# Performance work log

Measured on AMD Instinct MI355X. Metric: run time of the kernel, lower is better.

The kernel has to match this reference:

```python
import jax, jax.numpy as jnp
import numpy as np

N, E, D, G, L = 100_000, 500_000, 128, 512, 4
BN_EPS = 1e-5

def _bn(v, g, b):
    # BatchNorm1d in training mode: biased batch stats over node/graph axis
    m = v.mean(0)
    var = v.var(0)
    return (v - m) * jax.lax.rsqrt(var + BN_EPS) * g + b

def setup_inputs() -> dict:
    key = jax.random.key(0)
    ks = jax.random.split(key, 12)
    s = 0.05
    return {
        "x": jax.random.normal(ks[0], (N, D), jnp.float32),
        "edge_index": jax.random.randint(ks[1], (2, E), 0, N, jnp.int64),
        "batch": jnp.sort(jax.random.randint(ks[2], (N,), 0, G, jnp.int64)),
        "num_graphs": G,
        "W1": jax.random.normal(ks[3], (L, D, 2 * D), jnp.float32) * s,
        "b1": jnp.zeros((L, 2 * D), jnp.float32),
        "g1": jnp.ones((L, 2 * D), jnp.float32),
        "be1": jnp.zeros((L, 2 * D), jnp.float32),
        "W2": jax.random.normal(ks[4], (L, 2 * D, D), jnp.float32) * s,
        "b2": jnp.zeros((L, D), jnp.float32),
        "gbn": jnp.ones((L, D), jnp.float32),
        "bbn": jnp.zeros((L, D), jnp.float32),
        "eps": jnp.zeros((L,), jnp.float32),
        "cW1": jax.random.normal(ks[5], (3 * D, D), jnp.float32) * s,
        "cb1": jnp.zeros((D,), jnp.float32),
        "cg": jnp.ones((D,), jnp.float32),
        "cbeta": jnp.zeros((D,), jnp.float32),
        "cW2": jax.random.normal(ks[6], (D, D // 2), jnp.float32) * s,
        "cb2": jnp.zeros((D // 2,), jnp.float32),
        "cW3": jax.random.normal(ks[7], (D // 2, 2), jnp.float32) * s,
        "cb3": jnp.zeros((2,), jnp.float32),
    }

def reference(x, edge_index, batch, num_graphs, W1, b1, g1, be1, W2, b2, gbn, bbn, eps,
              cW1, cb1, cg, cbeta, cW2, cb2, cW3, cb3):
    n = x.shape[0]
    src, dst = edge_index[0], edge_index[1]
    for l in range(W1.shape[0]):
        # GINConv: mlp((1+eps)*x + sum_{j in N(i)} x_j)  (scatter-add to dst)
        agg = jax.ops.segment_sum(x[src], dst, num_segments=n)
        h = (1.0 + eps[l]) * x + agg
        h = jax.nn.relu(_bn(h @ W1[l] + b1[l], g1[l], be1[l]))
        h = h @ W2[l] + b2[l]
        x = jax.nn.relu(_bn(h, gbn[l], bbn[l]))  # outer BN + ReLU (dropout off: eval)
    # multi-pool readout: add / mean / max per graph
    s = jax.ops.segment_sum(x, batch, num_segments=num_graphs)
    cnt = jax.ops.segment_sum(jnp.ones((n,), x.dtype), batch, num_segments=num_graphs)
    mean = s / jnp.maximum(cnt, 1.0)[:, None]
    mx = jax.ops.segment_max(x, batch, num_segments=num_graphs)
    z = jnp.concatenate([s, mean, mx], axis=-1)  # [G, 3*D]
    z = jax.nn.relu(_bn(z @ cW1 + cb1, cg, cbeta))
    z = jax.nn.relu(z @ cW2 + cb2)
    return z @ cW3 + cb3
```

## Files before the change

### kernel.cpp

```cpp
#include <hip/hip_runtime.h>
#include <cstdint>
#include <cstddef>

#define NN 100000
#define EE 500000
#define DD 128
#define GG 512
#define LL 4
#define BN_EPS 1e-5f

typedef __attribute__((ext_vector_type(8))) short short8;
typedef __attribute__((ext_vector_type(8))) unsigned short ushort8v;
typedef __attribute__((ext_vector_type(4))) float f32x4;

static __device__ __forceinline__ unsigned short f2bf(float f) {
  union { float f; unsigned u; } v;
  v.f = f;
  unsigned r = v.u + 0x7fffu + ((v.u >> 16) & 1u);
  return (unsigned short)(r >> 16);
}
static __device__ __forceinline__ float bf2f(unsigned short u) {
  union { unsigned u; float f; } v;
  v.u = ((unsigned)u) << 16;
  return v.f;
}


__global__ void k_hist(const int* __restrict__ ei, int* __restrict__ cnt) {
  int e = blockIdx.x * 256 + threadIdx.x;
  if (e < EE) {
    int d = ei[EE + e];
    if (d >= 0 && d < NN) atomicAdd(&cnt[d], 1);
  }
}

__global__ void k_part(const int* __restrict__ cnt, int* __restrict__ part) {
  __shared__ int sm[1024];
  int t = threadIdx.x;
  int i = blockIdx.x * 1024 + t;
  sm[t] = (i < NN) ? cnt[i] : 0;
  __syncthreads();
  for (int off = 512; off > 0; off >>= 1) {
    if (t < off) sm[t] += sm[t + off];
    __syncthreads();
  }
  if (t == 0) part[blockIdx.x] = sm[0];
}

__global__ void k_scanpart(const int* __restrict__ part, int* __restrict__ partx, int nb) {
  __shared__ int sm[128];
  int t = threadIdx.x;
  int v = (t < nb) ? part[t] : 0;
  sm[t] = v;
  __syncthreads();
  for (int off = 1; off < 128; off <<= 1) {
    int u = (t >= off) ? sm[t - off] : 0;
    __syncthreads();
    sm[t] += u;
    __syncthreads();
  }
  if (t < nb) partx[t] = sm[t] - v;
}

__global__ void k_rs(const int* __restrict__ cnt, const int* __restrict__ partx,
                     int* __restrict__ rs, int* __restrict__ cur) {
  __shared__ int sm[1024];
  int t = threadIdx.x;
  int i = blockIdx.x * 1024 + t;
  int v = (i < NN) ? cnt[i] : 0;
  sm[t] = v;
  __syncthreads();
  for (int off = 1; off < 1024; off <<= 1) {
    int u = (t >= off) ? sm[t - off] : 0;
    __syncthreads();
    sm[t] += u;
    __syncthreads();
  }
  if (i < NN) {
    int excl = partx[blockIdx.x] + sm[t] - v;
    rs[i] = excl;
    cur[i] = excl;
    if (i == NN - 1) rs[NN] = excl + v;
  }
}

__global__ void k_fill(const int* __restrict__ ei, int* __restrict__ cur,
                       int* __restrict__ ci) {
  int e = blockIdx.x * 256 + threadIdx.x;
  if (e < EE) {
    int s = ei[e];
    int d = ei[EE + e];
    if (d >= 0 && d < NN && s >= 0 && s < NN) {
      int pos = atomicAdd(&cur[d], 1);
      if (pos >= 0 && pos < EE) ci[pos] = s;
    }
  }
}


__global__ void k_conv(const float* __restrict__ W1, const float* __restrict__ W2,
                       unsigned short* __restrict__ W1t, unsigned short* __restrict__ W2t) {
  int idx = blockIdx.x * 256 + threadIdx.x;
  if (idx < 4 * 256 * 128) {
    {
      int l = idx >> 15, rem = idx & 32767;
      int nc = rem >> 7, k = rem & 127;
      W1t[idx] = f2bf(W1[(l << 15) + k * 256 + nc]);
    }
    {
      int l = idx >> 15, rem = idx & 32767;
      int nc = rem >> 8, k = rem & 255;
      W2t[idx] = f2bf(W2[(l << 15) + k * 128 + nc]);
    }
  }
}


__global__ void k_x2bf(const float* __restrict__ x, unsigned short* __restrict__ xb) {
  int i = blockIdx.x * 256 + threadIdx.x;
  if (i < NN * DD / 4) {
    float4 v = *(const float4*)(x + (size_t)i * 4);
    ushort4 o;
    o.x = f2bf(v.x); o.y = f2bf(v.y); o.z = f2bf(v.z); o.w = f2bf(v.w);
    *(ushort4*)(xb + (size_t)i * 4) = o;
  }
}


__global__ __launch_bounds__(256) void k_agg_bf16(
    const unsigned short* __restrict__ X, const int* __restrict__ rs,
    const int* __restrict__ ci, const float* __restrict__ epsv, int l, int mode,
    const float* __restrict__ tsc, const float* __restrict__ tsh,
    unsigned short* __restrict__ h0, int n) {
  int idx = blockIdx.x * 256 + threadIdx.x;
  int node = idx >> 4;
  int c8 = (idx & 15) << 3;
  if (node >= n) return;
  float sa[8], sb[8];
  if (mode) {
    float4 a0 = *(const float4*)(tsc + c8), a1 = *(const float4*)(tsc + c8 + 4);
    float4 b0 = *(const float4*)(tsh + c8), b1 = *(const float4*)(tsh + c8 + 4);
    sa[0] = a0.x; sa[1] = a0.y; sa[2] = a0.z; sa[3] = a0.w;
    sa[4] = a1.x; sa[5] = a1.y; sa[6] = a1.z; sa[7] = a1.w;
    sb[0] = b0.x; sb[1] = b0.y; sb[2] = b0.z; sb[3] = b0.w;
    sb[4] = b1.x; sb[5] = b1.y; sb[6] = b1.z; sb[7] = b1.w;
  }
  float se = 1.f + epsv[l];
  ushort8v v = *(const ushort8v*)(X + (size_t)node * DD + c8);
  float acc[8];
#pragma unroll
  for (int j = 0; j < 8; ++j) {
    float f = bf2f(v[j]);
    if (mode) f = fmaxf(0.f, f * sa[j] + sb[j]);
    acc[j] = se * f;
  }
  int e0 = rs[node], e1 = rs[node + 1];
  ushort8v un;
  if (e0 < e1) un = *(const ushort8v*)(X + (size_t)ci[e0] * DD + c8);
  for (int e = e0; e < e1; ++e) {
    ushort8v uc = un;
    if (e + 1 < e1) un = *(const ushort8v*)(X + (size_t)ci[e + 1] * DD + c8);
#pragma unroll
    for (int j = 0; j < 8; ++j) {
      float f = bf2f(uc[j]);
      if (mode) f = fmaxf(0.f, f * sa[j] + sb[j]);
      acc[j] += f;
    }
  }
  ushort8v o;
#pragma unroll
  for (int j = 0; j < 8; ++j) o[j] = f2bf(acc[j]);
  *(ushort8v*)(h0 + (size_t)node * DD + c8) = o;
}


template <int K, int NC>
__global__ __launch_bounds__(512) void k_gemm(
    const unsigned short* __restrict__ A, int mode, const float* __restrict__ tsc,
    const float* __restrict__ tsh, const unsigned short* __restrict__ Bt,
    const float* __restrict__ bias, unsigned short* __restrict__ C,
    float* __restrict__ psum, float* __restrict__ psq, int n) {
  constexpr int KC = 64;
  constexpr int KT = K / KC;
  constexpr int NT = NC / 128;
  constexpr int P = KT * NT;
  constexpr int AST = 72;
  constexpr int CTP = 136;
  __shared__ __align__(16) unsigned short smem[2 * 128 * AST];
  __shared__ float bsum[128], bsq[128];
  unsigned short* Asm = smem;
  unsigned short* Bsm = smem + 128 * AST;
  unsigned short* Ct = smem;

  int tid = threadIdx.x;
  int lane = tid & 63, wave = tid >> 6;
  int quad = lane >> 4, l15 = lane & 15;
  int row0 = blockIdx.x * 128;
  int blk = blockIdx.x;

  ushort8v pa[2], pb[2];
#pragma unroll
  for (int it = 0; it < 2; ++it) {
    int f = tid + it * 512;
    int r = f >> 3;
    int c8 = (f & 7) << 3;
    int gr = row0 + r;
    pa[it] = (ushort8v){0, 0, 0, 0, 0, 0, 0, 0};
    if (gr < n) pa[it] = *(const ushort8v*)(A + (size_t)gr * K + c8);
    pb[it] = *(const ushort8v*)(Bt + (size_t)r * K + c8);
  }

  f32x4 acc[8];
  for (int p = 0; p < P; ++p) {
    int cg = p / KT, kc = p % KT;
    if (kc == 0) {
#pragma unroll
      for (int j = 0; j < 8; ++j) acc[j] = (f32x4){0.f, 0.f, 0.f, 0.f};
    }
#pragma unroll
    for (int it = 0; it < 2; ++it) {
      int f = tid + it * 512;
      int r = f >> 3;
      int c8 = (f & 7) << 3;
      ushort8v v = pa[it];
      if (mode) {
        int kg = kc * KC + c8;
        float4 s0 = *(const float4*)(tsc + kg);
        float4 s1 = *(const float4*)(tsc + kg + 4);
        float4 t0 = *(const float4*)(tsh + kg);
        float4 t1 = *(const float4*)(tsh + kg + 4);
        float sa[8] = {s0.x, s0.y, s0.z, s0.w, s1.x, s1.y, s1.z, s1.w};
        float sb[8] = {t0.x, t0.y, t0.z, t0.w, t1.x, t1.y, t1.z, t1.w};
#pragma unroll
        for (int j = 0; j < 8; ++j)
          v[j] = f2bf(fmaxf(0.f, bf2f(v[j]) * sa[j] + sb[j]));
      }
      *(ushort8v*)(&Asm[r * AST + c8]) = v;
      *(ushort8v*)(&Bsm[r * AST + c8]) = pb[it];
    }
    __syncthreads();
    if (p + 1 < P) {
      int cg2 = (p + 1) / KT, kc2 = (p + 1) % KT;
#pragma unroll
      for (int it = 0; it < 2; ++it) {
        int f = tid + it * 512;
        int r = f >> 3;
        int c8 = (f & 7) << 3;
        int gr = row0 + r;
        pa[it] = (ushort8v){0, 0, 0, 0, 0, 0, 0, 0};
        if (gr < n) pa[it] = *(const ushort8v*)(A + (size_t)gr * K + kc2 * KC + c8);
        pb[it] = *(const ushort8v*)(Bt + (size_t)(cg2 * 128 + r) * K + kc2 * KC + c8);
      }
    }
#pragma unroll
    for (int kk = 0; kk < KC; kk += 32) {
      int ko = kk + quad * 8;
      short8 av = *(const short8*)(&Asm[(wave * 16 + l15) * AST + ko]);
#pragma unroll
      for (int cf = 0; cf < 8; ++cf) {
        short8 bv = *(const short8*)(&Bsm[(cf * 16 + l15) * AST + ko]);
        acc[cf] = __builtin_amdgcn_mfma_f32_16x16x32_bf16(av, bv, acc[cf], 0, 0, 0);
      }
    }
    if (kc == KT - 1) {
      __syncthreads();
      if (tid < 128) { bsum[tid] = 0.f; bsq[tid] = 0.f; }
      float s8[8], q8[8];
#pragma unroll
      for (int j = 0; j < 8; ++j) { s8[j] = 0.f; q8[j] = 0.f; }
      int lrbase = wave * 16 + quad * 4;
#pragma unroll
      for (int cf = 0; cf < 8; ++cf) {
        int col = cg * 128 + cf * 16 + l15;
        float bv = bias[col];
#pragma unroll
        for (int reg = 0; reg < 4; ++reg) {
          int lr = lrbase + reg;
          float e = acc[cf][reg] + bv;
          Ct[lr * CTP + cf * 16 + l15] = f2bf(e);
          if (row0 + lr < n) { s8[cf] += e; q8[cf] += e * e; }
        }
      }
#pragma unroll
      for (int cf = 0; cf < 8; ++cf) {
        s8[cf] += __shfl_xor(s8[cf], 16, 64);
        s8[cf] += __shfl_xor(s8[cf], 32, 64);
        q8[cf] += __shfl_xor(q8[cf], 16, 64);
        q8[cf] += __shfl_xor(q8[cf], 32, 64);
      }
      __syncthreads();
      if (quad == 0) {
#pragma unroll
        for (int cf = 0; cf < 8; ++cf) {
          atomicAdd(&bsum[cf * 16 + l15], s8[cf]);
          atomicAdd(&bsq[cf * 16 + l15], q8[cf]);
        }
      }
#pragma unroll
      for (int it = 0; it < 4; ++it) {
        int f = tid + it * 512;
        int r = f >> 4;
        int c8 = (f & 15) << 3;
        int gr = row0 + r;
        if (gr < n)
          *(ushort8v*)(C + (size_t)gr * NC + cg * 128 + c8) =
              *(const ushort8v*)(&Ct[r * CTP + c8]);
      }
      __syncthreads();
      if (tid < 128) {
        psum[(size_t)blk * NC + cg * 128 + tid] = bsum[tid];
        psq[(size_t)blk * NC + cg * 128 + tid] = bsq[tid];
      }
    } else {
      __syncthreads();
    }
  }
}


__global__ __launch_bounds__(256) void k_finred(
    const float* __restrict__ psum, const float* __restrict__ psq, int nb, int nc,
    const float* __restrict__ g, const float* __restrict__ be,
    float* __restrict__ osc, float* __restrict__ osh, float invn) {
  __shared__ float ws[4], wq[4];
  int col = blockIdx.x;
  int t = threadIdx.x;
  float s = 0.f, q = 0.f;
  for (int b = t; b < nb; b += 256) {
    s += psum[(size_t)b * nc + col];
    q += psq[(size_t)b * nc + col];
  }
#pragma unroll
  for (int off = 32; off > 0; off >>= 1) {
    s += __shfl_xor(s, off, 64);
    q += __shfl_xor(q, off, 64);
  }
  if ((t & 63) == 0) { ws[t >> 6] = s; wq[t >> 6] = q; }
  __syncthreads();
  if (t == 0) {
    s = ws[0] + ws[1] + ws[2] + ws[3];
    q = wq[0] + wq[1] + wq[2] + wq[3];
    float m = s * invn;
    float v = fmaxf(q * invn - m * m, 0.f);
    float sc = g[col] * rsqrtf(v + BN_EPS);
    osc[col] = sc;
    osh[col] = be[col] - m * sc;
  }
}


__global__ __launch_bounds__(256) void k_statz(
    const float* __restrict__ z1, const float* __restrict__ g,
    const float* __restrict__ be, float* __restrict__ osc, float* __restrict__ osh) {
  __shared__ float ws[4], wq[4];
  int col = blockIdx.x;
  int t = threadIdx.x;
  float s = 0.f, q = 0.f;
  for (int b = t; b < GG; b += 256) {
    float v = z1[(size_t)b * 128 + col];
    s += v;
    q += v * v;
  }
#pragma unroll
  for (int off = 32; off > 0; off >>= 1) {
    s += __shfl_xor(s, off, 64);
    q += __shfl_xor(q, off, 64);
  }
  if ((t & 63) == 0) { ws[t >> 6] = s; wq[t >> 6] = q; }
  __syncthreads();
  if (t == 0) {
    s = ws[0] + ws[1] + ws[2] + ws[3];
    q = wq[0] + wq[1] + wq[2] + wq[3];
    float m = s / (float)GG;
    float v = fmaxf(q / (float)GG - m * m, 0.f);
    float sc = g[col] * rsqrtf(v + BN_EPS);
    osc[col] = sc;
    osh[col] = be[col] - m * sc;
  }
}


static __device__ __forceinline__ int lb_i32(const int* a, int n, int key) {
  int lo = 0, hi = n;
  while (lo < hi) {
    int mid = (lo + hi) >> 1;
    if (a[mid] < key) lo = mid + 1; else hi = mid;
  }
  return lo;
}

__global__ __launch_bounds__(512) void k_pool(
    const unsigned short* __restrict__ X, const int* __restrict__ batch,
    const float* __restrict__ tsc, const float* __restrict__ tsh,
    float* __restrict__ z, int n) {
  __shared__ int slo, shi;
  __shared__ float ssum[8][128], smax[8][128];
  int g = blockIdx.x;
  int t = threadIdx.x;
  int sg = t >> 6;
  int c2 = (t & 63) << 1;
  if (t == 0) {
    slo = lb_i32(batch, n, g);
    shi = lb_i32(batch, n, g + 1);
  }
  __syncthreads();
  int lo = slo, hi = shi;
  float a0 = tsc[c2], a1 = tsc[c2 + 1];
  float b0 = tsh[c2], b1 = tsh[c2 + 1];
  float s0 = 0.f, s1 = 0.f;
  float m0 = -3.402823466e38f, m1 = -3.402823466e38f;
  for (int i = lo + sg; i < hi; i += 8) {
    unsigned u = *(const unsigned*)(X + (size_t)i * DD + c2);
    float v0 = fmaxf(0.f, bf2f((unsigned short)(u & 0xffff)) * a0 + b0);
    float v1 = fmaxf(0.f, bf2f((unsigned short)(u >> 16)) * a1 + b1);
    s0 += v0; m0 = fmaxf(m0, v0);
    s1 += v1; m1 = fmaxf(m1, v1);
  }
  ssum[sg][c2] = s0; ssum[sg][c2 + 1] = s1;
  smax[sg][c2] = m0; smax[sg][c2 + 1] = m1;
  __syncthreads();
  if (t < 128) {
    float S = 0.f, M = -3.402823466e38f;
#pragma unroll
    for (int k = 0; k < 8; ++k) {
      S += ssum[k][t];
      M = fmaxf(M, smax[k][t]);
    }
    float cntf = (float)(hi - lo);
    z[(size_t)g * 384 + t] = S;
    z[(size_t)g * 384 + 128 + t] = S / fmaxf(cntf, 1.f);
    z[(size_t)g * 384 + 256 + t] = M;
  }
}


__global__ void k_cls1(const float* __restrict__ z, const float* __restrict__ cW1,
                       const float* __restrict__ cb1, float* __restrict__ z1) {
  __shared__ float zr[384];
  int g = blockIdx.x;
  int c = threadIdx.x;
  for (int i = c; i < 384; i += 128) zr[i] = z[(size_t)g * 384 + i];
  __syncthreads();
  float s = cb1[c];
#pragma unroll 4
  for (int k = 0; k < 384; ++k) s = fmaf(zr[k], cW1[(size_t)k * 128 + c], s);
  z1[(size_t)g * 128 + c] = s;
}

__global__ void k_cls2(const float* __restrict__ z1, const float* __restrict__ csc,
                       const float* __restrict__ csh, const float* __restrict__ cW2,
                       const float* __restrict__ cb2, const float* __restrict__ cW3,
                       const float* __restrict__ cb3, float* __restrict__ out) {
  __shared__ float z1n[128];
  __shared__ float z2s[64];
  int g = blockIdx.x;
  int t = threadIdx.x;
  z1n[t] = fmaxf(0.f, z1[(size_t)g * 128 + t] * csc[t] + csh[t]);
  __syncthreads();
  if (t < 64) {
    float s = cb2[t];
#pragma unroll 4
    for (int k = 0; k < 128; ++k) s = fmaf(z1n[k], cW2[(size_t)k * 64 + t], s);
    z2s[t] = fmaxf(0.f, s);
  }
  __syncthreads();
  if (t < 2) {
    float s = cb3[t];
#pragma unroll 4
    for (int c = 0; c < 64; ++c) s = fmaf(z2s[c], cW3[(size_t)c * 2 + t], s);
    out[(size_t)g * 2 + t] = s;
  }
}


extern "C" void kernel_launch(void* const* d_in, const int* in_sizes, int n_in,
                              void* d_out, int out_size, void* d_ws, size_t ws_size,
                              hipStream_t stream) {
  const float* x = (const float*)d_in[0];
  const int* ei = (const int*)d_in[1];
  const int* batch = (const int*)d_in[2];
  const float* W1 = (const float*)d_in[4];
  const float* b1 = (const float*)d_in[5];
  const float* g1 = (const float*)d_in[6];
  const float* be1 = (const float*)d_in[7];
  const float* W2 = (const float*)d_in[8];
  const float* b2 = (const float*)d_in[9];
  const float* gbn = (const float*)d_in[10];
  const float* bbn = (const float*)d_in[11];
  const float* epsv = (const float*)d_in[12];
  const float* cW1 = (const float*)d_in[13];
  const float* cb1 = (const float*)d_in[14];
  const float* cg = (const float*)d_in[15];
  const float* cbeta = (const float*)d_in[16];
  const float* cW2 = (const float*)d_in[17];
  const float* cb2 = (const float*)d_in[18];
  const float* cW3 = (const float*)d_in[19];
  const float* cb3 = (const float*)d_in[20];
  float* out = (float*)d_out;

  char* p = (char*)d_ws;
  auto alloc = [&](size_t bytes) {
    char* r = p;
    p += (bytes + 255) & ~(size_t)255;
    return r;
  };
  const int NB = (NN + 127) / 128;
  int* cnt = (int*)alloc((size_t)NN * 4);
  int* rs = (int*)alloc((size_t)(NN + 1) * 4);
  int* cur = (int*)alloc((size_t)NN * 4);
  int* ci = (int*)alloc((size_t)EE * 4);
  int* part = (int*)alloc(128 * 4);
  int* partx = (int*)alloc(128 * 4);
  unsigned short* xbf = (unsigned short*)alloc((size_t)NN * DD * 2);
  unsigned short* h0 = (unsigned short*)alloc((size_t)NN * DD * 2);
  unsigned short* h1 = (unsigned short*)alloc((size_t)NN * 2 * DD * 2);
  unsigned short* xp = (unsigned short*)alloc((size_t)NN * DD * 2);
  float* psum = (float*)alloc((size_t)NB * 256 * 4);
  float* psq = (float*)alloc((size_t)NB * 256 * 4);
  float* tsc1 = (float*)alloc(256 * 4);
  float* tsh1 = (float*)alloc(256 * 4);
  float* tscX = (float*)alloc(128 * 4);
  float* tshX = (float*)alloc(128 * 4);
  float* zbuf = (float*)alloc((size_t)GG * 384 * 4);
  float* z1 = (float*)alloc((size_t)GG * 128 * 4);
  unsigned short* W1t = (unsigned short*)alloc((size_t)4 * 256 * 128 * 2);
  unsigned short* W2t = (unsigned short*)alloc((size_t)4 * 128 * 256 * 2);
  (void)ws_size; (void)n_in; (void)in_sizes; (void)out_size;

  k_conv<<<512, 256, 0, stream>>>(W1, W2, W1t, W2t);
  k_x2bf<<<(NN * DD / 4 + 255) / 256, 256, 0, stream>>>(x, xbf);

  hipMemsetAsync(cnt, 0, (size_t)NN * 4, stream);
  k_hist<<<(EE + 255) / 256, 256, 0, stream>>>(ei, cnt);
  const int nscan = (NN + 1023) / 1024;
  k_part<<<nscan, 1024, 0, stream>>>(cnt, part);
  k_scanpart<<<1, 128, 0, stream>>>(part, partx, nscan);
  k_rs<<<nscan, 1024, 0, stream>>>(cnt, partx, rs, cur);
  k_fill<<<(EE + 255) / 256, 256, 0, stream>>>(ei, cur, ci);

  for (int l = 0; l < LL; ++l) {
    const unsigned short* Xl = (l == 0) ? xbf : xp;
    k_agg_bf16<<<(NN * 16 + 255) / 256, 256, 0, stream>>>(
        Xl, rs, ci, epsv, l, (l > 0) ? 1 : 0, tscX, tshX, h0, NN);
    k_gemm<128, 256><<<NB, 512, 0, stream>>>(
        h0, 0, nullptr, nullptr, W1t + (size_t)l * 256 * 128,
        b1 + (size_t)l * 256, h1, psum, psq, NN);
    k_finred<<<256, 256, 0, stream>>>(psum, psq, NB, 256, g1 + (size_t)l * 256,
                                      be1 + (size_t)l * 256, tsc1, tsh1, 1.0f / NN);
    k_gemm<256, 128><<<NB, 512, 0, stream>>>(
        h1, 1, tsc1, tsh1, W2t + (size_t)l * 128 * 256,
        b2 + (size_t)l * 128, xp, psum, psq, NN);
    k_finred<<<128, 256, 0, stream>>>(psum, psq, NB, 128, gbn + (size_t)l * 128,
                                      bbn + (size_t)l * 128, tscX, tshX, 1.0f / NN);
  }

  k_pool<<<GG, 512, 0, stream>>>(xp, batch, tscX, tshX, zbuf, NN);
  k_cls1<<<GG, 128, 0, stream>>>(zbuf, cW1, cb1, z1);
  k_statz<<<128, 256, 0, stream>>>(z1, cg, cbeta, tscX, tshX);
  k_cls2<<<GG, 128, 0, stream>>>(z1, tscX, tshX, cW2, cb2, cW3, cb3, out);
}
```

Before: 764.8 us.

## Recompute first GEMM in fused kernel instead of storing intermediate activations

```diff
diff --git a/kernel.cpp b/kernel.cpp
--- a/kernel.cpp
+++ b/kernel.cpp
@@ -174,146 +174,235 @@
 }
 
 
-template <int K, int NC>
-__global__ __launch_bounds__(512) void k_gemm(
-    const unsigned short* __restrict__ A, int mode, const float* __restrict__ tsc,
-    const float* __restrict__ tsh, const unsigned short* __restrict__ Bt,
-    const float* __restrict__ bias, unsigned short* __restrict__ C,
-    float* __restrict__ psum, float* __restrict__ psq, int n) {
-  constexpr int KC = 64;
-  constexpr int KT = K / KC;
-  constexpr int NT = NC / 128;
-  constexpr int P = KT * NT;
-  constexpr int AST = 72;
-  constexpr int CTP = 136;
-  __shared__ __align__(16) unsigned short smem[2 * 128 * AST];
+__global__ __launch_bounds__(512) void k_gstat(
+    const unsigned short* __restrict__ A, const unsigned short* __restrict__ Bt,
+    const float* __restrict__ bias, float* __restrict__ psum,
+    float* __restrict__ psq, int n) {
+  constexpr int AST = 136;
+  __shared__ __align__(16) unsigned short As[128 * AST];
+  __shared__ __align__(16) unsigned short Bs[128 * AST];
   __shared__ float bsum[128], bsq[128];
-  unsigned short* Asm = smem;
-  unsigned short* Bsm = smem + 128 * AST;
-  unsigned short* Ct = smem;
-
   int tid = threadIdx.x;
   int lane = tid & 63, wave = tid >> 6;
   int quad = lane >> 4, l15 = lane & 15;
   int row0 = blockIdx.x * 128;
   int blk = blockIdx.x;
 
-  ushort8v pa[2], pb[2];
-#pragma unroll
-  for (int it = 0; it < 2; ++it) {
+#pragma unroll
+  for (int it = 0; it < 4; ++it) {
     int f = tid + it * 512;
-    int r = f >> 3;
-    int c8 = (f & 7) << 3;
+    int r = f >> 4;
+    int c8 = (f & 15) << 3;
     int gr = row0 + r;
-    pa[it] = (ushort8v){0, 0, 0, 0, 0, 0, 0, 0};
-    if (gr < n) pa[it] = *(const ushort8v*)(A + (size_t)gr * K + c8);
-    pb[it] = *(const ushort8v*)(Bt + (size_t)r * K + c8);
-  }
-
-  f32x4 acc[8];
-  for (int p = 0; p < P; ++p) {
-    int cg = p / KT, kc = p % KT;
-    if (kc == 0) {
-#pragma unroll
-      for (int j = 0; j < 8; ++j) acc[j] = (f32x4){0.f, 0.f, 0.f, 0.f};
-    }
-#pragma unroll
-    for (int it = 0; it < 2; ++it) {
+    ushort8v v = (ushort8v){0, 0, 0, 0, 0, 0, 0, 0};
+    if (gr < n) v = *(const ushort8v*)(A + (size_t)gr * 128 + c8);
+    *(ushort8v*)(&As[r * AST + c8]) = v;
+  }
+
+  for (int cg = 0; cg < 2; ++cg) {
+#pragma unroll
+    for (int it = 0; it < 4; ++it) {
       int f = tid + it * 512;
-      int r = f >> 3;
-      int c8 = (f & 7) << 3;
-      ushort8v v = pa[it];
-      if (mode) {
-        int kg = kc * KC + c8;
-        float4 s0 = *(const float4*)(tsc + kg);
-        float4 s1 = *(const float4*)(tsc + kg + 4);
-        float4 t0 = *(const float4*)(tsh + kg);
-        float4 t1 = *(const float4*)(tsh + kg + 4);
-        float sa[8] = {s0.x, s0.y, s0.z, s0.w, s1.x, s1.y, s1.z, s1.w};
-        float sb[8] = {t0.x, t0.y, t0.z, t0.w, t1.x, t1.y, t1.z, t1.w};
-#pragma unroll
-        for (int j = 0; j < 8; ++j)
-          v[j] = f2bf(fmaxf(0.f, bf2f(v[j]) * sa[j] + sb[j]));
-      }
-      *(ushort8v*)(&Asm[r * AST + c8]) = v;
-      *(ushort8v*)(&Bsm[r * AST + c8]) = pb[it];
-    }
-    __syncthreads();
-    if (p + 1 < P) {
-      int cg2 = (p + 1) / KT, kc2 = (p + 1) % KT;
-#pragma unroll
-      for (int it = 0; it < 2; ++it) {
-        int f = tid + it * 512;
-        int r = f >> 3;
-        int c8 = (f & 7) << 3;
-        int gr = row0 + r;
-        pa[it] = (ushort8v){0, 0, 0, 0, 0, 0, 0, 0};
-        if (gr < n) pa[it] = *(const ushort8v*)(A + (size_t)gr * K + kc2 * KC + c8);
-        pb[it] = *(const ushort8v*)(Bt + (size_t)(cg2 * 128 + r) * K + kc2 * KC + c8);
-      }
-    }
-#pragma unroll
-    for (int kk = 0; kk < KC; kk += 32) {
+      int r = f >> 4;
+      int c8 = (f & 15) << 3;
+      *(ushort8v*)(&Bs[r * AST + c8]) =
+          *(const ushort8v*)(Bt + (size_t)(cg * 128 + r) * 128 + c8);
+    }
+    if (tid < 128) { bsum[tid] = 0.f; bsq[tid] = 0.f; }
+    __syncthreads();
+
+    f32x4 acc[8];
+#pragma unroll
+    for (int j = 0; j < 8; ++j) acc[j] = (f32x4){0.f, 0.f, 0.f, 0.f};
+#pragma unroll
+    for (int kk = 0; kk < 128; kk += 32) {
       int ko = kk + quad * 8;
-      short8 av = *(const short8*)(&Asm[(wave * 16 + l15) * AST + ko]);
+      short8 av = *(const short8*)(&As[(wave * 16 + l15) * AST + ko]);
 #pragma unroll
       for (int cf = 0; cf < 8; ++cf) {
-        short8 bv = *(const short8*)(&Bsm[(cf * 16 + l15) * AST + ko]);
+        short8 bv = *(const short8*)(&Bs[(cf * 16 + l15) * AST + ko]);
         acc[cf] = __builtin_amdgcn_mfma_f32_16x16x32_bf16(av, bv, acc[cf], 0, 0, 0);
       }
     }
-    if (kc == KT - 1) {
-      __syncthreads();
-      if (tid < 128) { bsum[tid] = 0.f; bsq[tid] = 0.f; }
-      float s8[8], q8[8];
-#pragma unroll
-      for (int j = 0; j < 8; ++j) { s8[j] = 0.f; q8[j] = 0.f; }
-      int lrbase = wave * 16 + quad * 4;
-#pragma unroll
-      for (int cf = 0; cf < 8; ++cf) {
-        int col = cg * 128 + cf * 16 + l15;
-        float bv = bias[col];
-#pragma unroll
-        for (int reg = 0; reg < 4; ++reg) {
-          int lr = lrbase + reg;
+    float s8[8], q8[8];
+#pragma unroll
+    for (int j = 0; j < 8; ++j) { s8[j] = 0.f; q8[j] = 0.f; }
+    int lrbase = wave * 16 + quad * 4;
+#pragma unroll
+    for (int cf = 0; cf < 8; ++cf) {
+      float bv = bias[cg * 128 + cf * 16 + l15];
+#pragma unroll
+      for (int reg = 0; reg < 4; ++reg) {
+        if (row0 + lrbase + reg < n) {
           float e = acc[cf][reg] + bv;
-          Ct[lr * CTP + cf * 16 + l15] = f2bf(e);
-          if (row0 + lr < n) { s8[cf] += e; q8[cf] += e * e; }
+          s8[cf] += e;
+          q8[cf] += e * e;
         }
       }
+    }
+#pragma unroll
+    for (int cf = 0; cf < 8; ++cf) {
+      s8[cf] += __shfl_xor(s8[cf], 16, 64);
+      s8[cf] += __shfl_xor(s8[cf], 32, 64);
+      q8[cf] += __shfl_xor(q8[cf], 16, 64);
+      q8[cf] += __shfl_xor(q8[cf], 32, 64);
+    }
+    if (quad == 0) {
 #pragma unroll
       for (int cf = 0; cf < 8; ++cf) {
-        s8[cf] += __shfl_xor(s8[cf], 16, 64);
-        s8[cf] += __shfl_xor(s8[cf], 32, 64);
-        q8[cf] += __shfl_xor(q8[cf], 16, 64);
-        q8[cf] += __shfl_xor(q8[cf], 32, 64);
+        atomicAdd(&bsum[cf * 16 + l15], s8[cf]);
+        atomicAdd(&bsq[cf * 16 + l15], q8[cf]);
       }
-      __syncthreads();
-      if (quad == 0) {
-#pragma unroll
-        for (int cf = 0; cf < 8; ++cf) {
-          atomicAdd(&bsum[cf * 16 + l15], s8[cf]);
-          atomicAdd(&bsq[cf * 16 + l15], q8[cf]);
-        }
+    }
+    __syncthreads();
+    if (tid < 128) {
+      psum[(size_t)blk * 256 + cg * 128 + tid] = bsum[tid];
+      psq[(size_t)blk * 256 + cg * 128 + tid] = bsq[tid];
+    }
+  }
+}
+
+
+__global__ __launch_bounds__(512) void k_fused(
+    const unsigned short* __restrict__ A, const unsigned short* __restrict__ B1t,
+    const float* __restrict__ b1, const float* __restrict__ tsc1,
+    const float* __restrict__ tsh1, const unsigned short* __restrict__ B2t,
+    const float* __restrict__ b2, unsigned short* __restrict__ C,
+    float* __restrict__ psum, float* __restrict__ psq, int n) {
+  constexpr int AST = 136;
+  constexpr int HST = 264;
+  __shared__ __align__(16) unsigned short As[128 * AST];
+  __shared__ __align__(16) unsigned short Ws[128 * AST];
+  __shared__ __align__(16) unsigned short Ht[128 * HST];
+  __shared__ float bsum[128], bsq[128];
+  int tid = threadIdx.x;
+  int lane = tid & 63, wave = tid >> 6;
+  int quad = lane >> 4, l15 = lane & 15;
+  int row0 = blockIdx.x * 128;
+  int blk = blockIdx.x;
+
+#pragma unroll
+  for (int it = 0; it < 4; ++it) {
+    int f = tid + it * 512;
+    int r = f >> 4;
+    int c8 = (f & 15) << 3;
+    int gr = row0 + r;
+    ushort8v v = (ushort8v){0, 0, 0, 0, 0, 0, 0, 0};
+    if (gr < n) v = *(const ushort8v*)(A + (size_t)gr * 128 + c8);
+    *(ushort8v*)(&As[r * AST + c8]) = v;
+  }
+
+  for (int cg = 0; cg < 2; ++cg) {
+#pragma unroll
+    for (int it = 0; it < 4; ++it) {
+      int f = tid + it * 512;
+      int r = f >> 4;
+      int c8 = (f & 15) << 3;
+      *(ushort8v*)(&Ws[r * AST + c8]) =
+          *(const ushort8v*)(B1t + (size_t)(cg * 128 + r) * 128 + c8);
+    }
+    if (cg == 0 && tid < 128) { bsum[tid] = 0.f; bsq[tid] = 0.f; }
+    __syncthreads();
+
+    f32x4 acc[8];
+#pragma unroll
+    for (int j = 0; j < 8; ++j) acc[j] = (f32x4){0.f, 0.f, 0.f, 0.f};
+#pragma unroll
+    for (int kk = 0; kk < 128; kk += 32) {
+      int ko = kk + quad * 8;
+      short8 av = *(const short8*)(&As[(wave * 16 + l15) * AST + ko]);
+#pragma unroll
+      for (int cf = 0; cf < 8; ++cf) {
+        short8 bv = *(const short8*)(&Ws[(cf * 16 + l15) * AST + ko]);
+        acc[cf] = __builtin_amdgcn_mfma_f32_16x16x32_bf16(av, bv, acc[cf], 0, 0, 0);
       }
-#pragma unroll
-      for (int it = 0; it < 4; ++it) {
-        int f = tid + it * 512;
-        int r = f >> 4;
-        int c8 = (f & 15) << 3;
-        int gr = row0 + r;
-        if (gr < n)
-          *(ushort8v*)(C + (size_t)gr * NC + cg * 128 + c8) =
-              *(const ushort8v*)(&Ct[r * CTP + c8]);
+    }
+    int lrbase = wave * 16 + quad * 4;
+#pragma unroll
+    for (int cf = 0; cf < 8; ++cf) {
+      int col = cg * 128 + cf * 16 + l15;
+      float bv = b1[col];
+      float sc = tsc1[col], sh = tsh1[col];
+#pragma unroll
+      for (int reg = 0; reg < 4; ++reg) {
+        float e = acc[cf][reg] + bv;
+        float hn = fmaxf(0.f, e * sc + sh);
+        Ht[(lrbase + reg) * HST + col] = f2bf(hn);
       }
-      __syncthreads();
-      if (tid < 128) {
-        psum[(size_t)blk * NC + cg * 128 + tid] = bsum[tid];
-        psq[(size_t)blk * NC + cg * 128 + tid] = bsq[tid];
+    }
+    __syncthreads();
+  }
+
+  f32x4 acc2[8];
+#pragma unroll
+  for (int j = 0; j < 8; ++j) acc2[j] = (f32x4){0.f, 0.f, 0.f, 0.f};
+  for (int kc = 0; kc < 2; ++kc) {
+#pragma unroll
+    for (int it = 0; it < 4; ++it) {
+      int f = tid + it * 512;
+      int r = f >> 4;
+      int c8 = (f & 15) << 3;
+      *(ushort8v*)(&Ws[r * AST + c8]) =
+          *(const ushort8v*)(B2t + (size_t)r * 256 + kc * 128 + c8);
+    }
+    __syncthreads();
+#pragma unroll
+    for (int kk = 0; kk < 128; kk += 32) {
+      int ko = kk + quad * 8;
+      short8 av = *(const short8*)(&Ht[(wave * 16 + l15) * HST + kc * 128 + ko]);
+#pragma unroll
+      for (int cf = 0; cf < 8; ++cf) {
+        short8 bv = *(const short8*)(&Ws[(cf * 16 + l15) * AST + ko]);
+        acc2[cf] = __builtin_amdgcn_mfma_f32_16x16x32_bf16(av, bv, acc2[cf], 0, 0, 0);
       }
-    } else {
-      __syncthreads();
-    }
+    }
+    __syncthreads();
+  }
+
+  unsigned short* Ct = As;
+  float s8[8], q8[8];
+#pragma unroll
+  for (int j = 0; j < 8; ++j) { s8[j] = 0.f; q8[j] = 0.f; }
+  int lrbase = wave * 16 + quad * 4;
+#pragma unroll
+  for (int cf = 0; cf < 8; ++cf) {
+    int col = cf * 16 + l15;
+    float bv = b2[col];
+#pragma unroll
+    for (int reg = 0; reg < 4; ++reg) {
+      int lr = lrbase + reg;
+      float e = acc2[cf][reg] + bv;
+      Ct[lr * AST + col] = f2bf(e);
+      if (row0 + lr < n) { s8[cf] += e; q8[cf] += e * e; }
+    }
+  }
+#pragma unroll
+  for (int cf = 0; cf < 8; ++cf) {
+    s8[cf] += __shfl_xor(s8[cf], 16, 64);
+    s8[cf] += __shfl_xor(s8[cf], 32, 64);
+    q8[cf] += __shfl_xor(q8[cf], 16, 64);
+    q8[cf] += __shfl_xor(q8[cf], 32, 64);
+  }
+  if (quad == 0) {
+#pragma unroll
+    for (int cf = 0; cf < 8; ++cf) {
+      atomicAdd(&bsum[cf * 16 + l15], s8[cf]);
+      atomicAdd(&bsq[cf * 16 + l15], q8[cf]);
+    }
+  }
+  __syncthreads();
+#pragma unroll
+  for (int it = 0; it < 4; ++it) {
+    int f = tid + it * 512;
+    int r = f >> 4;
+    int c8 = (f & 15) << 3;
+    int gr = row0 + r;
+    if (gr < n)
+      *(ushort8v*)(C + (size_t)gr * 128 + c8) = *(const ushort8v*)(&Ct[r * AST + c8]);
+  }
+  if (tid < 128) {
+    psum[(size_t)blk * 128 + tid] = bsum[tid];
+    psq[(size_t)blk * 128 + tid] = bsq[tid];
   }
 }
 
@@ -513,7 +602,6 @@
   int* partx = (int*)alloc(128 * 4);
   unsigned short* xbf = (unsigned short*)alloc((size_t)NN * DD * 2);
   unsigned short* h0 = (unsigned short*)alloc((size_t)NN * DD * 2);
-  unsigned short* h1 = (unsigned short*)alloc((size_t)NN * 2 * DD * 2);
   unsigned short* xp = (unsigned short*)alloc((size_t)NN * DD * 2);
   float* psum = (float*)alloc((size_t)NB * 256 * 4);
   float* psq = (float*)alloc((size_t)NB * 256 * 4);
@@ -542,14 +630,14 @@
     const unsigned short* Xl = (l == 0) ? xbf : xp;
     k_agg_bf16<<<(NN * 16 + 255) / 256, 256, 0, stream>>>(
         Xl, rs, ci, epsv, l, (l > 0) ? 1 : 0, tscX, tshX, h0, NN);
-    k_gemm<128, 256><<<NB, 512, 0, stream>>>(
-        h0, 0, nullptr, nullptr, W1t + (size_t)l * 256 * 128,
-        b1 + (size_t)l * 256, h1, psum, psq, NN);
+    k_gstat<<<NB, 512, 0, stream>>>(h0, W1t + (size_t)l * 256 * 128,
+                                    b1 + (size_t)l * 256, psum, psq, NN);
     k_finred<<<256, 256, 0, stream>>>(psum, psq, NB, 256, g1 + (size_t)l * 256,
                                       be1 + (size_t)l * 256, tsc1, tsh1, 1.0f / NN);
-    k_gemm<256, 128><<<NB, 512, 0, stream>>>(
-        h1, 1, tsc1, tsh1, W2t + (size_t)l * 128 * 256,
-        b2 + (size_t)l * 128, xp, psum, psq, NN);
+    k_fused<<<NB, 512, 0, stream>>>(h0, W1t + (size_t)l * 256 * 128,
+                                    b1 + (size_t)l * 256, tsc1, tsh1,
+                                    W2t + (size_t)l * 128 * 256,
+                                    b2 + (size_t)l * 128, xp, psum, psq, NN);
     k_finred<<<128, 256, 0, stream>>>(psum, psq, NB, 128, gbn + (size_t)l * 128,
                                       bbn + (size_t)l * 128, tscX, tshX, 1.0f / NN);
   }
```

Result: slower. 819.1 us (+7.1%).
